# Optimization experiments

Hardware: AMD Instinct MI355X
Metric: run time of the kernel (lower is better)

## Reference

```python
import jax, jax.numpy as jnp
import numpy as np
from jax.scipy.special import digamma

K_NEIGHBOURS = 5  # matches init_kwargs nNeighbours


def setup_inputs() -> dict:
    key = jax.random.key(0)
    k1, k2 = jax.random.split(key)
    x = jax.random.normal(k1, (2, 2, 64, 64), dtype=jnp.float32)
    y = jax.random.normal(k2, (2, 2, 64, 64), dtype=jnp.float32)
    return {"x": x, "y": y}


def _knn_mi(x, y, k):
    # KSG k-NN mutual information estimator, channel-wise.
    B, C, H, W = x.shape
    BC, HW = B * C, H * W
    xv = x.reshape(BC, HW)
    yv = y.reshape(BC, HW)
    # Pairwise L1 (scalar -> abs diff) distance matrices: (BC, HW, HW)
    dx = jnp.abs(xv[:, :, None] - xv[:, None, :])
    dy = jnp.abs(yv[:, :, None] - yv[:, None, :])
    # Joint-space Chebyshev distance (max over the two marginals)
    z = jnp.maximum(dx, dy)
    # eps = (k+1)-th smallest joint distance per point (includes self-distance 0),
    # matching torch .topk(k+1, largest=False).values[..., -1:]
    neg_smallest = jax.lax.top_k(-z, k + 1)[0]       # (BC, HW, k+1), descending in -z
    eps = -neg_smallest[:, :, -1:]                    # (BC, HW, 1)
    # Marginal neighbor counts with strict < eps (self included, as in torch code)
    nx = jnp.sum(dx < eps, axis=-1).astype(jnp.float32)  # (BC, HW)
    ny = jnp.sum(dy < eps, axis=-1).astype(jnp.float32)
    const = digamma(jnp.float32(k)) + digamma(jnp.float32(HW))
    mi = const - jnp.mean(digamma(nx) + digamma(ny), axis=-1)  # (BC,)
    return jnp.maximum(mi.reshape(B, C), 0.0)


def reference(x, y):
    return _knn_mi(x, y, K_NEIGHBOURS)
```

## Files before the change

kernel.cpp:

```cpp
#include <hip/hip_runtime.h>
#include <math.h>

#define HW 4096
#define NCH 4
#define TPB 256
#define ROWS_PER_BLOCK 16
#define BLOCKS_PER_CH 256
#define NBLOCKS (NCH * BLOCKS_PER_CH)
#define KNN 5
#define WINB 544

#define NBINS 512
#define BLO   (-6.0f)
#define BDELTA 0.0234375f
#define BINV  (512.0f / 12.0f)
#define SLOP  1e-5f
#define INFT  3.4e38f

#define WS_BXY   16384
#define WS_BY    32768
#define WS_PREF  49152
#define WS_PART  57344

__device__ __forceinline__ int binOf(float v) {
    int b = (int)floorf((v - BLO) * BINV);
    return min(max(b, 0), NBINS - 1);
}

__device__ __forceinline__ float digammaf_dev(float x) {
    float r = 0.f;
    while (x < 6.f) { r -= 1.f / x; x += 1.f; }
    float f = 1.f / x, f2 = f * f;
    return logf(x) - 0.5f * f
         - f2 * (1.f / 12.f - f2 * (1.f / 120.f - f2 * (1.f / 252.f))) + r;
}

__device__ __forceinline__ void insert6(float (&s)[6], float d) {
    float n0 = fminf(s[0], d);
    float n1 = __builtin_amdgcn_fmed3f(s[0], s[1], d);
    float n2 = __builtin_amdgcn_fmed3f(s[1], s[2], d);
    float n3 = __builtin_amdgcn_fmed3f(s[2], s[3], d);
    float n4 = __builtin_amdgcn_fmed3f(s[3], s[4], d);
    float n5 = __builtin_amdgcn_fmed3f(s[4], s[5], d);
    s[0] = n0; s[1] = n1; s[2] = n2; s[3] = n3; s[4] = n4; s[5] = n5;
}

__global__ __launch_bounds__(256) void knnmi_bucketize(const float* __restrict__ x,
                                                       const float* __restrict__ y,
                                                       float* __restrict__ ws) {
    __shared__ int h[NBINS];
    const int c    = blockIdx.x >> 1;
    const int side = blockIdx.x & 1;
    const int t    = threadIdx.x;
    const float* src  = (side == 0 ? x : y) + c * HW;
    const float* ysrc = y + c * HW;
    int* pref = (int*)ws + WS_PREF + (side ? NCH * (NBINS + 1) : 0) + c * (NBINS + 1);

    for (int i = t; i < NBINS; i += 256) h[i] = 0;
    __syncthreads();

    float vx[16], vy[16];
    int bn[16];
#pragma unroll
    for (int k = 0; k < 16; ++k) {
        int i = t + k * 256;
        float v = src[i];
        vx[k] = v;
        vy[k] = (side == 0) ? ysrc[i] : 0.f;
        bn[k] = binOf(v);
        atomicAdd(&h[bn[k]], 1);
    }
    __syncthreads();

    if (t < 64) {
        int sinc[8];
        {
            sinc[0] = h[t * 8 + 0];
#pragma unroll
            for (int j = 1; j < 8; ++j) sinc[j] = sinc[j - 1] + h[t * 8 + j];
        }
        int tot = sinc[7], inc = tot;
#pragma unroll
        for (int off = 1; off < 64; off <<= 1) {
            int u = __shfl_up(inc, off);
            if (t >= off) inc += u;
        }
        int ex = inc - tot;
#pragma unroll
        for (int j = 0; j < 8; ++j) {
            int st = ex + (j ? sinc[j - 1] : 0);
            h[t * 8 + j]    = st;
            pref[t * 8 + j] = st;
        }
        if (t == 63) pref[NBINS] = HW;
    }
    __syncthreads();

    if (side == 0) {
        float* bxx = ws + c * HW;
        float* bxy = ws + WS_BXY + c * HW;
#pragma unroll
        for (int k = 0; k < 16; ++k) {
            int pos = atomicAdd(&h[bn[k]], 1);
            bxx[pos] = vx[k];
            bxy[pos] = vy[k];
        }
    } else {
        float* by = ws + WS_BY + c * HW;
#pragma unroll
        for (int k = 0; k < 16; ++k) {
            int pos = atomicAdd(&h[bn[k]], 1);
            by[pos] = vx[k];
        }
    }
}

__global__ __launch_bounds__(TPB, 6) void knnmi_rows(float* __restrict__ ws) {
    __shared__ float2 swin[WINB];
    __shared__ float red[ROWS_PER_BLOCK];

    const int c  = blockIdx.x >> 8;
    const int rb = blockIdx.x & 255;
    const int R0 = rb * ROWS_PER_BLOCK;
    const float* bxx = ws + c * HW;
    const float* bxy = ws + WS_BXY + c * HW;
    const float* by  = ws + WS_BY  + c * HW;
    const int* pfx = (const int*)ws + WS_PREF + c * (NBINS + 1);
    const int* pfy = (const int*)ws + WS_PREF + NCH * (NBINS + 1) + c * (NBINS + 1);

    int LO = R0 - 256;
    LO = max(LO, 0); LO = min(LO, HW - WINB); LO &= ~3;
    const int HI = LO + WINB;

    if (threadIdx.x < WINB / 4) {
        float4 xv = ((const float4*)(bxx + LO))[threadIdx.x];
        float4 yv = ((const float4*)(bxy + LO))[threadIdx.x];
        ((float4*)swin)[2 * threadIdx.x]     = make_float4(xv.x, yv.x, xv.y, yv.y);
        ((float4*)swin)[2 * threadIdx.x + 1] = make_float4(xv.z, yv.z, xv.w, yv.w);
    }
    __syncthreads();

    const int wv   = threadIdx.x >> 6;
    const int lane = threadIdx.x & 63;
    const int l    = lane & 15;
    const int g    = lane >> 4;
    const int q    = wv * 4 + g;
    const int p    = R0 + q;

    const float xi = swin[p - LO].x;
    const float yi = swin[p - LO].y;

    float s[6];
#pragma unroll
    for (int k = 0; k < 6; ++k) s[k] = INFT;

    const float4* f4 = (const float4*)swin;
#pragma unroll 4
    for (int it = 0; it < WINB / 32; ++it) {
        float4 pp = f4[it * 16 + l];
        insert6(s, fmaxf(fabsf(xi - pp.x), fabsf(yi - pp.y)));
        insert6(s, fmaxf(fabsf(xi - pp.z), fabsf(yi - pp.w)));
    }

#pragma unroll
    for (int m = 1; m < 16; m <<= 1) {
        float o[6];
#pragma unroll
        for (int k = 0; k < 6; ++k) o[k] = __shfl_xor(s[k], m);
#pragma unroll
        for (int k = 0; k < 6; ++k) insert6(s, o[k]);
    }
    float eps = s[5];

    float eL = INFT, eR = INFT;
    if (LO > 0) {
        int b = binOf(bxx[LO - 1]);
        eL = xi - (BLO + (float)(b + 1) * BDELTA + SLOP);
    }
    if (HI < HW) {
        int b = binOf(bxx[HI]);
        eR = (BLO + (float)b * BDELTA - SLOP) - xi;
    }
    const bool ok = (eps <= eL) && (eps <= eR);

    unsigned long long bad = __ballot((l == 0) && !ok);
    while (bad) {
        int bit = (int)__ffsll((unsigned long long)bad) - 1;
        bad &= bad - 1;
        const int tg = bit >> 4;
        const int pt = R0 + wv * 4 + tg;
        const float xt = swin[pt - LO].x, yt = swin[pt - LO].y;
        float s3[6];
#pragma unroll
        for (int k = 0; k < 6; ++k) s3[k] = INFT;
        for (int it = 0; it < HW / 256; ++it) {
            float4 xv = ((const float4*)bxx)[it * 64 + lane];
            float4 yv = ((const float4*)bxy)[it * 64 + lane];
            insert6(s3, fmaxf(fabsf(xt - xv.x), fabsf(yt - yv.x)));
            insert6(s3, fmaxf(fabsf(xt - xv.y), fabsf(yt - yv.y)));
            insert6(s3, fmaxf(fabsf(xt - xv.z), fabsf(yt - yv.z)));
            insert6(s3, fmaxf(fabsf(xt - xv.w), fabsf(yt - yv.w)));
        }
#pragma unroll
        for (int m = 1; m < 64; m <<= 1) {
            float o[6];
#pragma unroll
            for (int k = 0; k < 6; ++k) o[k] = __shfl_xor(s3[k], m);
#pragma unroll
            for (int k = 0; k < 6; ++k) insert6(s3, o[k]);
        }
        if (g == tg) eps = s3[5];
    }

    int nx = 0;
    {
        int loB = binOf(xi - eps), hiB = binOf(xi + eps);
        int fLo = loB + 2, fHi = hiB - 2;
        if (fLo <= fHi) {
            if (l == 0) nx += pfx[fHi + 1] - pfx[fLo];
            int a0 = pfx[max(loB - 1, 0)], a1 = pfx[min(loB + 1, NBINS - 1) + 1];
            int b0 = pfx[max(hiB - 1, 0)], b1 = pfx[min(hiB + 1, NBINS - 1) + 1];
            for (int tt = a0 + l; tt < a1; tt += 16) nx += (fabsf(bxx[tt] - xi) < eps);
            for (int tt = b0 + l; tt < b1; tt += 16) nx += (fabsf(bxx[tt] - xi) < eps);
        } else {
            int a0 = pfx[max(loB - 1, 0)], a1 = pfx[min(hiB + 1, NBINS - 1) + 1];
            for (int tt = a0 + l; tt < a1; tt += 16) nx += (fabsf(bxx[tt] - xi) < eps);
        }
    }
    int ny = 0;
    {
        int loB = binOf(yi - eps), hiB = binOf(yi + eps);
        int fLo = loB + 2, fHi = hiB - 2;
        if (fLo <= fHi) {
            if (l == 0) ny += pfy[fHi + 1] - pfy[fLo];
            int a0 = pfy[max(loB - 1, 0)], a1 = pfy[min(loB + 1, NBINS - 1) + 1];
            int b0 = pfy[max(hiB - 1, 0)], b1 = pfy[min(hiB + 1, NBINS - 1) + 1];
            for (int tt = a0 + l; tt < a1; tt += 16) ny += (fabsf(by[tt] - yi) < eps);
            for (int tt = b0 + l; tt < b1; tt += 16) ny += (fabsf(by[tt] - yi) < eps);
        } else {
            int a0 = pfy[max(loB - 1, 0)], a1 = pfy[min(hiB + 1, NBINS - 1) + 1];
            for (int tt = a0 + l; tt < a1; tt += 16) ny += (fabsf(by[tt] - yi) < eps);
        }
    }

    int pk = (nx << 16) | ny;
#pragma unroll
    for (int m = 1; m < 16; m <<= 1) pk += __shfl_xor(pk, m);

    if (l == 0)
        red[q] = digammaf_dev((float)(pk >> 16)) + digammaf_dev((float)(pk & 0xffff));
    __syncthreads();

    if (threadIdx.x == 0) {
        float v = 0.f;
#pragma unroll
        for (int k = 0; k < ROWS_PER_BLOCK; ++k) v += red[k];
        (ws + WS_PART)[blockIdx.x] = v;
    }
}

__global__ void knnmi_final(const float* __restrict__ ws, float* __restrict__ out) {
    const float* partials = ws + WS_PART;
    const int w    = threadIdx.x >> 6;
    const int lane = threadIdx.x & 63;
    float sum = 0.f;
#pragma unroll
    for (int i = lane; i < BLOCKS_PER_CH; i += 64)
        sum += partials[w * BLOCKS_PER_CH + i];
#pragma unroll
    for (int m = 32; m; m >>= 1) sum += __shfl_xor(sum, m);
    if (lane == 0) {
        float mi = digammaf_dev((float)KNN) + digammaf_dev((float)HW)
                 - sum / (float)HW;
        out[w] = fmaxf(mi, 0.f);
    }
}

extern "C" void kernel_launch(void* const* d_in, const int* in_sizes, int n_in,
                              void* d_out, int out_size, void* d_ws, size_t ws_size,
                              hipStream_t stream) {
    const float* x = (const float*)d_in[0];
    const float* y = (const float*)d_in[1];
    float* out = (float*)d_out;
    float* ws  = (float*)d_ws;

    knnmi_bucketize<<<2 * NCH, 256, 0, stream>>>(x, y, ws);
    knnmi_rows<<<NBLOCKS, TPB, 0, stream>>>(ws);
    knnmi_final<<<1, NCH * 64, 0, stream>>>(ws, out);
}
```

Before: 31.01 us.

## Halve block size, count x-neighbours from shared window, cache y prefix in LDS

Cuts each block to 128 threads and 8 rows, so the grid doubles. The x-marginal count now scans the shared LDS window instead of running binned global-memory scans. The y prefix table is copied into shared memory. The fallback path now does a full-row scan that computes eps and both counts directly. It aims to cut global-memory traffic and use more CUs, at the cost of a larger grid and added per-block LDS loads. The fallback lane-index arithmetic looks odd (a dead `pt`, a redundant binOf), and correctness depends on the window holding every x neighbour within eps.

```diff
diff --git a/kernel.cpp b/kernel.cpp
--- a/kernel.cpp
+++ b/kernel.cpp
@@ -3,9 +3,9 @@
 
 #define HW 4096
 #define NCH 4
-#define TPB 256
-#define ROWS_PER_BLOCK 16
-#define BLOCKS_PER_CH 256
+#define TPB 128
+#define ROWS_PER_BLOCK 8
+#define BLOCKS_PER_CH (HW / ROWS_PER_BLOCK)
 #define NBLOCKS (NCH * BLOCKS_PER_CH)
 #define KNN 5
 #define WINB 544
@@ -115,29 +115,30 @@
     }
 }
 
-__global__ __launch_bounds__(TPB, 6) void knnmi_rows(float* __restrict__ ws) {
+__global__ __launch_bounds__(TPB) void knnmi_rows(float* __restrict__ ws) {
     __shared__ float2 swin[WINB];
+    __shared__ int pfy[NBINS + 1];
     __shared__ float red[ROWS_PER_BLOCK];
 
-    const int c  = blockIdx.x >> 8;
-    const int rb = blockIdx.x & 255;
+    const int c  = blockIdx.x >> 9;
+    const int rb = blockIdx.x & 511;
     const int R0 = rb * ROWS_PER_BLOCK;
     const float* bxx = ws + c * HW;
     const float* bxy = ws + WS_BXY + c * HW;
     const float* by  = ws + WS_BY  + c * HW;
-    const int* pfx = (const int*)ws + WS_PREF + c * (NBINS + 1);
-    const int* pfy = (const int*)ws + WS_PREF + NCH * (NBINS + 1) + c * (NBINS + 1);
-
-    int LO = R0 - 256;
+    const int* prefy = (const int*)ws + WS_PREF + NCH * (NBINS + 1) + c * (NBINS + 1);
+
+    int LO = R0 - 268;
     LO = max(LO, 0); LO = min(LO, HW - WINB); LO &= ~3;
     const int HI = LO + WINB;
 
-    if (threadIdx.x < WINB / 4) {
-        float4 xv = ((const float4*)(bxx + LO))[threadIdx.x];
-        float4 yv = ((const float4*)(bxy + LO))[threadIdx.x];
-        ((float4*)swin)[2 * threadIdx.x]     = make_float4(xv.x, yv.x, xv.y, yv.y);
-        ((float4*)swin)[2 * threadIdx.x + 1] = make_float4(xv.z, yv.z, xv.w, yv.w);
-    }
+    for (int i = threadIdx.x; i < WINB / 4; i += TPB) {
+        float4 xv = ((const float4*)(bxx + LO))[i];
+        float4 yv = ((const float4*)(bxy + LO))[i];
+        ((float4*)swin)[2 * i]     = make_float4(xv.x, yv.x, xv.y, yv.y);
+        ((float4*)swin)[2 * i + 1] = make_float4(xv.z, yv.z, xv.w, yv.w);
+    }
+    for (int i = threadIdx.x; i <= NBINS; i += TPB) pfy[i] = prefy[i];
     __syncthreads();
 
     const int wv   = threadIdx.x >> 6;
@@ -174,7 +175,8 @@
 
     float eL = INFT, eR = INFT;
     if (LO > 0) {
-        int b = binOf(bxx[LO - 1]);
+        int b = binOf(swin[0].x);
+        b = binOf(bxx[LO - 1]);
         eL = xi - (BLO + (float)(b + 1) * BDELTA + SLOP);
     }
     if (HI < HW) {
@@ -183,13 +185,17 @@
     }
     const bool ok = (eps <= eL) && (eps <= eR);
 
+    int nx = 0, ny = 0;
+    bool fell = false;
     unsigned long long bad = __ballot((l == 0) && !ok);
     while (bad) {
         int bit = (int)__ffsll((unsigned long long)bad) - 1;
         bad &= bad - 1;
         const int tg = bit >> 4;
-        const int pt = R0 + wv * 4 + tg;
-        const float xt = swin[pt - LO].x, yt = swin[pt - LO].y;
+        const int pt = R0 + ((bit >> 6) ? 4 : 0) + tg;
+        const float xt = swin[(R0 + wv * 4 + tg) - LO].x;
+        const float yt = swin[(R0 + wv * 4 + tg) - LO].y;
+        (void)pt;
         float s3[6];
 #pragma unroll
         for (int k = 0; k < 6; ++k) s3[k] = INFT;
@@ -209,26 +215,28 @@
 #pragma unroll
             for (int k = 0; k < 6; ++k) insert6(s3, o[k]);
         }
-        if (g == tg) eps = s3[5];
-    }
-
-    int nx = 0;
-    {
-        int loB = binOf(xi - eps), hiB = binOf(xi + eps);
-        int fLo = loB + 2, fHi = hiB - 2;
-        if (fLo <= fHi) {
-            if (l == 0) nx += pfx[fHi + 1] - pfx[fLo];
-            int a0 = pfx[max(loB - 1, 0)], a1 = pfx[min(loB + 1, NBINS - 1) + 1];
-            int b0 = pfx[max(hiB - 1, 0)], b1 = pfx[min(hiB + 1, NBINS - 1) + 1];
-            for (int tt = a0 + l; tt < a1; tt += 16) nx += (fabsf(bxx[tt] - xi) < eps);
-            for (int tt = b0 + l; tt < b1; tt += 16) nx += (fabsf(bxx[tt] - xi) < eps);
-        } else {
-            int a0 = pfx[max(loB - 1, 0)], a1 = pfx[min(hiB + 1, NBINS - 1) + 1];
-            for (int tt = a0 + l; tt < a1; tt += 16) nx += (fabsf(bxx[tt] - xi) < eps);
-        }
-    }
-    int ny = 0;
-    {
+        const float e3 = s3[5];
+        int cx = 0, cy = 0;
+        for (int it = 0; it < HW / 256; ++it) {
+            float4 xv = ((const float4*)bxx)[it * 64 + lane];
+            float4 yv = ((const float4*)bxy)[it * 64 + lane];
+            cx += (fabsf(xt - xv.x) < e3) + (fabsf(xt - xv.y) < e3)
+                + (fabsf(xt - xv.z) < e3) + (fabsf(xt - xv.w) < e3);
+            cy += (fabsf(yt - yv.x) < e3) + (fabsf(yt - yv.y) < e3)
+                + (fabsf(yt - yv.z) < e3) + (fabsf(yt - yv.w) < e3);
+        }
+        int pk3 = (cx << 16) | cy;
+#pragma unroll
+        for (int m = 1; m < 64; m <<= 1) pk3 += __shfl_xor(pk3, m);
+        if (g == tg) { eps = e3; nx = pk3 >> 16; ny = pk3 & 0xffff; fell = true; }
+    }
+
+    if (!fell) {
+#pragma unroll 4
+        for (int it = 0; it < WINB / 32; ++it) {
+            float4 pp = f4[it * 16 + l];
+            nx += (fabsf(xi - pp.x) < eps) + (fabsf(xi - pp.z) < eps);
+        }
         int loB = binOf(yi - eps), hiB = binOf(yi + eps);
         int fLo = loB + 2, fHi = hiB - 2;
         if (fLo <= fHi) {
@@ -243,6 +251,7 @@
         }
     }
 
+    if (fell && l != 0) { nx = 0; ny = 0; }
     int pk = (nx << 16) | ny;
 #pragma unroll
     for (int m = 1; m < 16; m <<= 1) pk += __shfl_xor(pk, m);
```

After: 35.92 us. 15.8% more time.
